# Kernel tuning notes

Measured on AMD Instinct MI355X. Metric: run time of the kernel, lower is better.

Reference implementation:

```python
import jax, jax.numpy as jnp
import numpy as np

B = 512    # batch of signals
N = 1024   # time samples per signal
M = 16384  # frequency grid points (super-resolved)


def setup_inputs() -> dict:
    key = jax.random.key(0)
    x = jax.random.normal(key, (B, 2, N), dtype=jnp.float32)  # [B, 2(re/im), N]
    xgrid = jnp.linspace(-0.5, 0.5, M, dtype=jnp.float32)      # normalized freqs
    return {"x": x, "xgrid": xgrid}


def reference(x, xgrid):
    # x: [B, 2, N] -> complex signal a + i*b
    # Periodogram at arbitrary freqs f: P(f) = |sum_n x_n * exp(-2j*pi*f*n)|^2 / N
    a = x[:, 0]  # real part [B, N]
    b = x[:, 1]  # imag part [B, N]
    Nn = x.shape[-1]
    n = jnp.arange(Nn, dtype=x.dtype)
    phase = (2.0 * jnp.pi) * xgrid[:, None] * n[None, :]  # [M, N]
    C = jnp.cos(phase)  # [M, N]
    S = jnp.sin(phase)  # [M, N]
    # x_n * (cos - i sin) = (a c + b s) + i (b c - a s)
    re = jnp.einsum('bn,mn->bm', a, C) + jnp.einsum('bn,mn->bm', b, S)
    im = jnp.einsum('bn,mn->bm', b, C) - jnp.einsum('bn,mn->bm', a, S)
    return (re * re + im * im) / Nn  # [B, M]
```

## Files before the change

kernel.cpp:

```cpp
#include <hip/hip_runtime.h>


typedef __fp16 half8  __attribute__((ext_vector_type(8)));
typedef __fp16 half2v __attribute__((ext_vector_type(2)));
typedef float  f32x4  __attribute__((ext_vector_type(4)));

#define B_SZ 512
#define N_SZ 1024
#define M_SZ 16384
#define BT 128
#define MT 128
#define KT 32
#define NT (N_SZ / KT)
#define WS_ARR 1048576

union U4 { half2v h2[4]; uint4 u; };
union BF { half2v h2[4]; half8 v; uint4 u; };

__device__ __forceinline__ void gld16(const void* g, void* l) {
    __builtin_amdgcn_global_load_lds((__attribute__((address_space(1))) void*)g,
                                     (__attribute__((address_space(3))) void*)l,
                                     16, 0, 0);
}

__global__ __launch_bounds__(256)
void cvt_kernel(const float* __restrict__ x, unsigned char* __restrict__ ws) {
    const int id  = (int)blockIdx.x * 256 + (int)threadIdx.x;
    const int arr = id >> 16;
    const int rem = id & 65535;
    const int rb  = rem >> 11;
    const int kc  = (rem >> 6) & 31;
    const int l6  = rem & 63;
    const int r16 = l6 >> 2;
    const int g   = l6 & 3;
    const float* src = x + (size_t)(rb * 16 + r16) * 2048 + arr * 1024 + kc * 32 + g * 8;
    const float4 v0 = *(const float4*)src;
    const float4 v1 = *(const float4*)(src + 4);
    U4 u;
    u.h2[0] = __builtin_amdgcn_cvt_pkrtz(v0.x, v0.y);
    u.h2[1] = __builtin_amdgcn_cvt_pkrtz(v0.z, v0.w);
    u.h2[2] = __builtin_amdgcn_cvt_pkrtz(v1.x, v1.y);
    u.h2[3] = __builtin_amdgcn_cvt_pkrtz(v1.z, v1.w);
    *(uint4*)(ws + (size_t)arr * WS_ARR + (size_t)(rb * 32 + kc) * 1024 + (g * 16 + r16) * 16) = u.u;
}

__global__ __launch_bounds__(256, 2)
void periodogram_kernel(const unsigned char* __restrict__ ws,
                        const float* __restrict__ xgrid,
                        float* __restrict__ out) {
    __shared__ __align__(16) unsigned char smem[65536];
    const int tid  = (int)threadIdx.x;
    const int lane = tid & 63;
    const int w    = tid >> 6;
    const int bid  = (int)blockIdx.x;
    const int b0 = (bid & 3) * BT;
    const int m0 = (bid >> 2) * MT;

    const int wr = (w >> 1) * 64;
    const int wc = (w & 1) * 64;

    unsigned char* lb = smem + (unsigned)(w * 16384);

    const unsigned char* pA[4];
    const unsigned char* pB[4];
#pragma unroll
    for (int fm = 0; fm < 4; ++fm) {
        const int rb = ((b0 + wr) >> 4) + fm;
        pA[fm] = ws + (size_t)(rb * 32) * 1024 + (size_t)(lane * 16);
        pB[fm] = pA[fm] + WS_ARR;
    }

    half2v PC[4][4], PS[4][4];
    float c0v[4], s0v[4], C32[4], S32[4];
    const float g8f = (float)((lane >> 4) << 3);
#pragma unroll
    for (int fn = 0; fn < 4; ++fn) {
        const float xg = xgrid[m0 + wc + fn * 16 + (lane & 15)];
        float Cj[8], Sj[8];
        Cj[0] = 1.0f; Sj[0] = 0.0f;
#pragma unroll
        for (int j = 1; j < 8; ++j) {
            float p = xg * (float)j; p -= floorf(p);
            Cj[j] = __builtin_amdgcn_cosf(p);
            Sj[j] = __builtin_amdgcn_sinf(p);
        }
#pragma unroll
        for (int i = 0; i < 4; ++i) {
            PC[fn][i] = __builtin_amdgcn_cvt_pkrtz(Cj[2 * i], Cj[2 * i + 1]);
            PS[fn][i] = __builtin_amdgcn_cvt_pkrtz(Sj[2 * i], Sj[2 * i + 1]);
        }
        float p32 = xg * 32.0f; p32 -= floorf(p32);
        C32[fn] = __builtin_amdgcn_cosf(p32);
        S32[fn] = __builtin_amdgcn_sinf(p32);
        float pb = xg * g8f; pb -= floorf(pb);
        c0v[fn] = __builtin_amdgcn_cosf(pb);
        s0v[fn] = __builtin_amdgcn_sinf(pb);
    }

    f32x4 accRe[4][4], accIm[4][4];
#pragma unroll
    for (int i = 0; i < 4; ++i)
#pragma unroll
        for (int j = 0; j < 4; ++j) { accRe[i][j] = (f32x4)0.0f; accIm[i][j] = (f32x4)0.0f; }

#pragma unroll
    for (int fm = 0; fm < 4; ++fm) {
        gld16(pA[fm], lb + (unsigned)(fm * 1024));
        gld16(pB[fm], lb + (unsigned)(4096 + fm * 1024));
    }

    for (int t = 0; t < NT; ++t) {
        const unsigned cb = (unsigned)(t & 1) * 8192u;
        asm volatile("s_waitcnt vmcnt(0)" ::: "memory");
        half8 fa[4], fb[4];
#pragma unroll
        for (int fm = 0; fm < 4; ++fm) {
            fa[fm] = *(const half8*)(lb + cb + (unsigned)(fm * 1024) + (unsigned)(lane * 16));
            fb[fm] = *(const half8*)(lb + cb + (unsigned)(4096 + fm * 1024) + (unsigned)(lane * 16));
        }
        if (t < NT - 1) {
            const unsigned nb = cb ^ 8192u;
            const unsigned off = (unsigned)((t + 1) * 1024);
#pragma unroll
            for (int fm = 0; fm < 4; ++fm) {
                gld16(pA[fm] + off, lb + nb + (unsigned)(fm * 1024));
                gld16(pB[fm] + off, lb + nb + (unsigned)(4096 + fm * 1024));
            }
        }
#pragma unroll
        for (int fn = 0; fn < 4; ++fn) {
            const float c0 = c0v[fn], s0 = s0v[fn];
            const half2v c0b = __builtin_amdgcn_cvt_pkrtz(c0, c0);
            const half2v s0b = __builtin_amdgcn_cvt_pkrtz(s0, s0);
            BF fc, fs, fns;
#pragma unroll
            for (int i = 0; i < 4; ++i) {
                fc.h2[i] = c0b * PC[fn][i] - s0b * PS[fn][i];
                fs.h2[i] = s0b * PC[fn][i] + c0b * PS[fn][i];
            }
            __builtin_amdgcn_s_setprio(1);
#pragma unroll
            for (int fm = 0; fm < 4; ++fm) {
                accRe[fm][fn] = __builtin_amdgcn_mfma_f32_16x16x32_f16(fa[fm], fc.v, accRe[fm][fn], 0, 0, 0);
                accIm[fm][fn] = __builtin_amdgcn_mfma_f32_16x16x32_f16(fb[fm], fc.v, accIm[fm][fn], 0, 0, 0);
            }
            fns.u.x = fs.u.x ^ 0x80008000u;
            fns.u.y = fs.u.y ^ 0x80008000u;
            fns.u.z = fs.u.z ^ 0x80008000u;
            fns.u.w = fs.u.w ^ 0x80008000u;
#pragma unroll
            for (int fm = 0; fm < 4; ++fm) {
                accRe[fm][fn] = __builtin_amdgcn_mfma_f32_16x16x32_f16(fb[fm], fs.v,  accRe[fm][fn], 0, 0, 0);
                accIm[fm][fn] = __builtin_amdgcn_mfma_f32_16x16x32_f16(fa[fm], fns.v, accIm[fm][fn], 0, 0, 0);
            }
            __builtin_amdgcn_s_setprio(0);
            c0v[fn] = __builtin_fmaf(c0, C32[fn], -(s0 * S32[fn]));
            s0v[fn] = __builtin_fmaf(s0, C32[fn],  (c0 * S32[fn]));
        }
    }

    const float inv = 1.0f / (float)N_SZ;
    const int orow0 = b0 + wr + ((lane >> 4) << 2);
    const int ocol0 = m0 + wc + (lane & 15);
#pragma unroll
    for (int fm = 0; fm < 4; ++fm)
#pragma unroll
        for (int fn = 0; fn < 4; ++fn) {
            const f32x4 r = accRe[fm][fn];
            const f32x4 im = accIm[fm][fn];
            const int col = ocol0 + fn * 16;
#pragma unroll
            for (int j = 0; j < 4; ++j) {
                const int row = orow0 + fm * 16 + j;
                out[(size_t)row * M_SZ + col] = (r[j] * r[j] + im[j] * im[j]) * inv;
            }
        }
}

extern "C" void kernel_launch(void* const* d_in, const int* in_sizes, int n_in,
                              void* d_out, int out_size, void* d_ws, size_t ws_size,
                              hipStream_t stream) {
    const float* x     = (const float*)d_in[0];
    const float* xgrid = (const float*)d_in[1];
    float* out = (float*)d_out;
    unsigned char* ws = (unsigned char*)d_ws;
    cvt_kernel<<<512, 256, 0, stream>>>(x, ws);
    dim3 grid(B_SZ / BT * (M_SZ / MT));
    dim3 block(256);
    periodogram_kernel<<<grid, block, 0, stream>>>(ws, xgrid, out);
}
```

Measured before the change: 66.94 us.

## Switch periodogram GEMM from 16x16x32 to 32x32x16 MFMA tiles

Replaces the 16x16x32 f16 MFMA tiling with 32x32x16 MFMAs over 2x2 fragments per wave. Each K=32 step is split into two K=16 halves, using an extra 16-step twiddle rotation (C16/S16). The A/B LDS load addressing and the output row/column mapping are remapped to fit the new operand layouts. The aim is fewer MFMA issues and fewer twiddle fragment builds per step, with better operand reuse. In exchange it adds a second rotated twiddle computation per step and riskier lane-to-data mapping.

```diff
diff --git a/kernel.cpp b/kernel.cpp
--- a/kernel.cpp
+++ b/kernel.cpp
@@ -3,7 +3,7 @@
 
 typedef __fp16 half8  __attribute__((ext_vector_type(8)));
 typedef __fp16 half2v __attribute__((ext_vector_type(2)));
-typedef float  f32x4  __attribute__((ext_vector_type(4)));
+typedef float  f32x16 __attribute__((ext_vector_type(16)));
 
 #define B_SZ 512
 #define N_SZ 1024
@@ -61,21 +61,23 @@
 
     unsigned char* lb = smem + (unsigned)(w * 16384);
 
-    const unsigned char* pA[4];
-    const unsigned char* pB[4];
-#pragma unroll
-    for (int fm = 0; fm < 4; ++fm) {
-        const int rb = ((b0 + wr) >> 4) + fm;
-        pA[fm] = ws + (size_t)(rb * 32) * 1024 + (size_t)(lane * 16);
-        pB[fm] = pA[fm] + WS_ARR;
+    const int l15 = lane & 15;
+    const int l45 = (lane >> 4) & 1;
+    const int l5  = lane >> 5;
+    const unsigned cellB = (unsigned)(((l5 << 4) + l15) << 4);
+    const unsigned char* pA[2];
+#pragma unroll
+    for (int fm = 0; fm < 2; ++fm) {
+        const int rb16 = ((b0 + wr) >> 4) + fm * 2 + l45;
+        pA[fm] = ws + (size_t)(rb16 * 32) * 1024 + cellB;
     }
 
-    half2v PC[4][4], PS[4][4];
-    float c0v[4], s0v[4], C32[4], S32[4];
-    const float g8f = (float)((lane >> 4) << 3);
-#pragma unroll
-    for (int fn = 0; fn < 4; ++fn) {
-        const float xg = xgrid[m0 + wc + fn * 16 + (lane & 15)];
+    half2v PC[2][4], PS[2][4];
+    float c0v[2], s0v[2], C16[2], S16[2], C32[2], S32[2];
+    const float g8f = (float)(l5 << 3);
+#pragma unroll
+    for (int fn = 0; fn < 2; ++fn) {
+        const float xg = xgrid[m0 + wc + fn * 32 + (lane & 31)];
         float Cj[8], Sj[8];
         Cj[0] = 1.0f; Sj[0] = 0.0f;
 #pragma unroll
@@ -89,6 +91,9 @@
             PC[fn][i] = __builtin_amdgcn_cvt_pkrtz(Cj[2 * i], Cj[2 * i + 1]);
             PS[fn][i] = __builtin_amdgcn_cvt_pkrtz(Sj[2 * i], Sj[2 * i + 1]);
         }
+        float p16 = xg * 16.0f; p16 -= floorf(p16);
+        C16[fn] = __builtin_amdgcn_cosf(p16);
+        S16[fn] = __builtin_amdgcn_sinf(p16);
         float p32 = xg * 32.0f; p32 -= floorf(p32);
         C32[fn] = __builtin_amdgcn_cosf(p32);
         S32[fn] = __builtin_amdgcn_sinf(p32);
@@ -97,61 +102,86 @@
         s0v[fn] = __builtin_amdgcn_sinf(pb);
     }
 
-    f32x4 accRe[4][4], accIm[4][4];
-#pragma unroll
-    for (int i = 0; i < 4; ++i)
-#pragma unroll
-        for (int j = 0; j < 4; ++j) { accRe[i][j] = (f32x4)0.0f; accIm[i][j] = (f32x4)0.0f; }
-
-#pragma unroll
-    for (int fm = 0; fm < 4; ++fm) {
-        gld16(pA[fm], lb + (unsigned)(fm * 1024));
-        gld16(pB[fm], lb + (unsigned)(4096 + fm * 1024));
-    }
+    f32x16 accRe[2][2], accIm[2][2];
+#pragma unroll
+    for (int i = 0; i < 2; ++i)
+#pragma unroll
+        for (int j = 0; j < 2; ++j) { accRe[i][j] = (f32x16)0.0f; accIm[i][j] = (f32x16)0.0f; }
+
+#pragma unroll
+    for (int fm = 0; fm < 2; ++fm)
+#pragma unroll
+        for (int kh = 0; kh < 2; ++kh) {
+            gld16(pA[fm] + kh * 512,          lb + (unsigned)((fm * 2 + kh) * 1024));
+            gld16(pA[fm] + WS_ARR + kh * 512, lb + (unsigned)(4096 + (fm * 2 + kh) * 1024));
+        }
 
     for (int t = 0; t < NT; ++t) {
         const unsigned cb = (unsigned)(t & 1) * 8192u;
         asm volatile("s_waitcnt vmcnt(0)" ::: "memory");
-        half8 fa[4], fb[4];
-#pragma unroll
-        for (int fm = 0; fm < 4; ++fm) {
-            fa[fm] = *(const half8*)(lb + cb + (unsigned)(fm * 1024) + (unsigned)(lane * 16));
-            fb[fm] = *(const half8*)(lb + cb + (unsigned)(4096 + fm * 1024) + (unsigned)(lane * 16));
-        }
+        half8 fa[2][2], fbb[2][2];
+#pragma unroll
+        for (int fm = 0; fm < 2; ++fm)
+#pragma unroll
+            for (int kh = 0; kh < 2; ++kh) {
+                fa[fm][kh]  = *(const half8*)(lb + cb + (unsigned)((fm * 2 + kh) * 1024) + (unsigned)(lane * 16));
+                fbb[fm][kh] = *(const half8*)(lb + cb + (unsigned)(4096 + (fm * 2 + kh) * 1024) + (unsigned)(lane * 16));
+            }
         if (t < NT - 1) {
             const unsigned nb = cb ^ 8192u;
             const unsigned off = (unsigned)((t + 1) * 1024);
 #pragma unroll
-            for (int fm = 0; fm < 4; ++fm) {
-                gld16(pA[fm] + off, lb + nb + (unsigned)(fm * 1024));
-                gld16(pB[fm] + off, lb + nb + (unsigned)(4096 + fm * 1024));
-            }
-        }
-#pragma unroll
-        for (int fn = 0; fn < 4; ++fn) {
+            for (int fm = 0; fm < 2; ++fm)
+#pragma unroll
+                for (int kh = 0; kh < 2; ++kh) {
+                    gld16(pA[fm] + off + kh * 512,          lb + nb + (unsigned)((fm * 2 + kh) * 1024));
+                    gld16(pA[fm] + WS_ARR + off + kh * 512, lb + nb + (unsigned)(4096 + (fm * 2 + kh) * 1024));
+                }
+        }
+#pragma unroll
+        for (int fn = 0; fn < 2; ++fn) {
             const float c0 = c0v[fn], s0 = s0v[fn];
             const half2v c0b = __builtin_amdgcn_cvt_pkrtz(c0, c0);
             const half2v s0b = __builtin_amdgcn_cvt_pkrtz(s0, s0);
-            BF fc, fs, fns;
+            BF fc0, fs0, fns0, fc1, fs1, fns1;
 #pragma unroll
             for (int i = 0; i < 4; ++i) {
-                fc.h2[i] = c0b * PC[fn][i] - s0b * PS[fn][i];
-                fs.h2[i] = s0b * PC[fn][i] + c0b * PS[fn][i];
-            }
+                fc0.h2[i] = c0b * PC[fn][i] - s0b * PS[fn][i];
+                fs0.h2[i] = s0b * PC[fn][i] + c0b * PS[fn][i];
+            }
+            const float c1 = __builtin_fmaf(c0, C16[fn], -(s0 * S16[fn]));
+            const float s1 = __builtin_fmaf(s0, C16[fn],  (c0 * S16[fn]));
+            const half2v c1b = __builtin_amdgcn_cvt_pkrtz(c1, c1);
+            const half2v s1b = __builtin_amdgcn_cvt_pkrtz(s1, s1);
+#pragma unroll
+            for (int i = 0; i < 4; ++i) {
+                fc1.h2[i] = c1b * PC[fn][i] - s1b * PS[fn][i];
+                fs1.h2[i] = s1b * PC[fn][i] + c1b * PS[fn][i];
+            }
+            fns0.u.x = fs0.u.x ^ 0x80008000u; fns0.u.y = fs0.u.y ^ 0x80008000u;
+            fns0.u.z = fs0.u.z ^ 0x80008000u; fns0.u.w = fs0.u.w ^ 0x80008000u;
+            fns1.u.x = fs1.u.x ^ 0x80008000u; fns1.u.y = fs1.u.y ^ 0x80008000u;
+            fns1.u.z = fs1.u.z ^ 0x80008000u; fns1.u.w = fs1.u.w ^ 0x80008000u;
             __builtin_amdgcn_s_setprio(1);
 #pragma unroll
-            for (int fm = 0; fm < 4; ++fm) {
-                accRe[fm][fn] = __builtin_amdgcn_mfma_f32_16x16x32_f16(fa[fm], fc.v, accRe[fm][fn], 0, 0, 0);
-                accIm[fm][fn] = __builtin_amdgcn_mfma_f32_16x16x32_f16(fb[fm], fc.v, accIm[fm][fn], 0, 0, 0);
-            }
-            fns.u.x = fs.u.x ^ 0x80008000u;
-            fns.u.y = fs.u.y ^ 0x80008000u;
-            fns.u.z = fs.u.z ^ 0x80008000u;
-            fns.u.w = fs.u.w ^ 0x80008000u;
-#pragma unroll
-            for (int fm = 0; fm < 4; ++fm) {
-                accRe[fm][fn] = __builtin_amdgcn_mfma_f32_16x16x32_f16(fb[fm], fs.v,  accRe[fm][fn], 0, 0, 0);
-                accIm[fm][fn] = __builtin_amdgcn_mfma_f32_16x16x32_f16(fa[fm], fns.v, accIm[fm][fn], 0, 0, 0);
+            for (int fm = 0; fm < 2; ++fm) {
+                accRe[fm][fn] = __builtin_amdgcn_mfma_f32_32x32x16_f16(fa[fm][0],  fc0.v, accRe[fm][fn], 0, 0, 0);
+                accIm[fm][fn] = __builtin_amdgcn_mfma_f32_32x32x16_f16(fbb[fm][0], fc0.v, accIm[fm][fn], 0, 0, 0);
+            }
+#pragma unroll
+            for (int fm = 0; fm < 2; ++fm) {
+                accRe[fm][fn] = __builtin_amdgcn_mfma_f32_32x32x16_f16(fa[fm][1],  fc1.v, accRe[fm][fn], 0, 0, 0);
+                accIm[fm][fn] = __builtin_amdgcn_mfma_f32_32x32x16_f16(fbb[fm][1], fc1.v, accIm[fm][fn], 0, 0, 0);
+            }
+#pragma unroll
+            for (int fm = 0; fm < 2; ++fm) {
+                accRe[fm][fn] = __builtin_amdgcn_mfma_f32_32x32x16_f16(fbb[fm][0], fs0.v,  accRe[fm][fn], 0, 0, 0);
+                accIm[fm][fn] = __builtin_amdgcn_mfma_f32_32x32x16_f16(fa[fm][0],  fns0.v, accIm[fm][fn], 0, 0, 0);
+            }
+#pragma unroll
+            for (int fm = 0; fm < 2; ++fm) {
+                accRe[fm][fn] = __builtin_amdgcn_mfma_f32_32x32x16_f16(fbb[fm][1], fs1.v,  accRe[fm][fn], 0, 0, 0);
+                accIm[fm][fn] = __builtin_amdgcn_mfma_f32_32x32x16_f16(fa[fm][1],  fns1.v, accIm[fm][fn], 0, 0, 0);
             }
             __builtin_amdgcn_s_setprio(0);
             c0v[fn] = __builtin_fmaf(c0, C32[fn], -(s0 * S32[fn]));
@@ -160,19 +190,18 @@
     }
 
     const float inv = 1.0f / (float)N_SZ;
-    const int orow0 = b0 + wr + ((lane >> 4) << 2);
-    const int ocol0 = m0 + wc + (lane & 15);
-#pragma unroll
-    for (int fm = 0; fm < 4; ++fm)
-#pragma unroll
-        for (int fn = 0; fn < 4; ++fn) {
-            const f32x4 r = accRe[fm][fn];
-            const f32x4 im = accIm[fm][fn];
-            const int col = ocol0 + fn * 16;
-#pragma unroll
-            for (int j = 0; j < 4; ++j) {
-                const int row = orow0 + fm * 16 + j;
-                out[(size_t)row * M_SZ + col] = (r[j] * r[j] + im[j] * im[j]) * inv;
+#pragma unroll
+    for (int fm = 0; fm < 2; ++fm)
+#pragma unroll
+        for (int fn = 0; fn < 2; ++fn) {
+            const f32x16 r = accRe[fm][fn];
+            const f32x16 im = accIm[fm][fn];
+            const int col = m0 + wc + fn * 32 + (lane & 31);
+            const int rowbase = b0 + wr + fm * 32 + (l5 << 2);
+#pragma unroll
+            for (int reg = 0; reg < 16; ++reg) {
+                const int row = rowbase + (reg & 3) + ((reg >> 2) << 3);
+                out[(size_t)row * M_SZ + col] = (r[reg] * r[reg] + im[reg] * im[reg]) * inv;
             }
         }
 }
```

Result: slower. 77.49 us (+15.8%).
